# Optimization experiments

Measured on AMD Instinct MI355X. Metric: run time of the kernel, lower is better.

Reference implementation:

```python
import jax, jax.numpy as jnp
import numpy as np


def setup_inputs() -> dict:
    key = jax.random.key(0)
    ks = jax.random.split(key, 12)
    N, F, H, E = 100000, 128, 128, 625000
    x = jax.random.normal(ks[0], (N, F), dtype=jnp.float32)
    edge_index = jax.random.randint(ks[1], (2, E), 0, N, dtype=jnp.int64)
    s1 = 1.0 / np.sqrt(2 * F)
    s2 = 1.0 / np.sqrt(H)
    W1 = jax.random.uniform(ks[2], (2 * F, H), jnp.float32, -s1, s1)
    b1 = jax.random.uniform(ks[3], (H,), jnp.float32, -s1, s1)
    W2 = jax.random.uniform(ks[4], (H, H), jnp.float32, -s2, s2)
    b2 = jax.random.uniform(ks[5], (H,), jnp.float32, -s2, s2)
    W3 = jax.random.uniform(ks[6], (H, H), jnp.float32, -s2, s2)
    b3 = jax.random.uniform(ks[7], (H,), jnp.float32, -s2, s2)
    W4 = jax.random.uniform(ks[8], (H, 1), jnp.float32, -s2, s2)
    b4 = jax.random.uniform(ks[9], (1,), jnp.float32, -s2, s2)
    return {"x": x, "edge_index": edge_index, "W1": W1, "b1": b1,
            "W2": W2, "b2": b2, "W3": W3, "b3": b3, "W4": W4, "b4": b4}


def reference(x, edge_index, W1, b1, W2, b2, W3, b3, W4, b4):
    # Gather endpoint features and concat -> [E, 2F]
    x_i = x[edge_index[0], :]
    x_j = x[edge_index[1], :]
    ef = jnp.concatenate([x_i, x_j], axis=-1)
    h = jax.nn.relu(ef @ W1 + b1)
    h = jax.nn.relu(h @ W2 + b2)
    h = jax.nn.relu(h @ W3 + b3)
    return jax.nn.sigmoid(h @ W4 + b4)  # [E, 1]
```

## Files before the change

### kernel.cpp

```cpp
#include <hip/hip_runtime.h>
#include <math.h>

typedef _Float16 half8 __attribute__((ext_vector_type(8)));
typedef _Float16 half4 __attribute__((ext_vector_type(4)));
typedef float f32x4 __attribute__((ext_vector_type(4)));

#define HDIM 128
#define WHALFS 65536
#define SCR_HALFS 2048
#define LDS_HALFS (WHALFS + 8 * SCR_HALFS)
#define LDS_BYTES (LDS_HALFS * 2)

__global__ __launch_bounds__(256) void prep_kernel(
    const float* __restrict__ x,  const float* __restrict__ W1,
    const float* __restrict__ W2, const float* __restrict__ W3,
    _Float16* __restrict__ xh,  _Float16* __restrict__ W1p,
    _Float16* __restrict__ W2p, _Float16* __restrict__ W3p, int NF)
{
    int bid = blockIdx.x;
    if (bid < 32) {
        int t = bid * 256 + threadIdx.x;
        const float* W; _Float16* Wp; int KS; int u;
        if (t < 4096)      { W = W1; Wp = W1p; KS = 8; u = t; }
        else if (t < 6144) { W = W2; Wp = W2p; KS = 4; u = t - 4096; }
        else               { W = W3; Wp = W3p; KS = 4; u = t - 6144; }
        int lane = u & 63;
        int fk   = u >> 6;
        int ks   = fk % KS;
        int ct   = fk / KS;
        int m    = ct * 16 + (lane & 15);
        int k0   = ks * 32 + (lane >> 4) * 8;
        half8 v;
        #pragma unroll
        for (int j = 0; j < 8; ++j) v[j] = (_Float16)W[(k0 + j) * HDIM + m];
        *(half8*)(Wp + (size_t)u * 8) = v;
    } else {
        long i = ((long)(bid - 32) * 256 + threadIdx.x) * 4;
        if (i + 4 <= (long)NF) {
            float4 f = *(const float4*)(x + i);
            half4 v;
            v[0] = (_Float16)f.x; v[1] = (_Float16)f.y;
            v[2] = (_Float16)f.z; v[3] = (_Float16)f.w;
            *(half4*)(xh + i) = v;
        }
    }
}

__device__ __forceinline__ void acc_bias_init(
    f32x4 (&acc)[2][8], const float* __restrict__ bias, int quad)
{
    #pragma unroll
    for (int ct = 0; ct < 8; ++ct) {
        float4 bv = *(const float4*)(bias + ct * 16 + quad * 4);
        f32x4 b = {bv.x, bv.y, bv.z, bv.w};
        acc[0][ct] = b;
        acc[1][ct] = b;
    }
}

__device__ __forceinline__ void epi_extract(
    f32x4 (&acc)[2][8], _Float16* __restrict__ scr, int l15, int quad, int sw,
    half8 (&bh)[2][4], const float* __restrict__ next_bias)
{
    #pragma unroll
    for (int nt = 0; nt < 2; ++nt) {
        #pragma unroll
        for (int ct = 0; ct < 8; ++ct) {
            half4 h;
            h[0] = (_Float16)fmaxf(acc[nt][ct][0], 0.f);
            h[1] = (_Float16)fmaxf(acc[nt][ct][1], 0.f);
            h[2] = (_Float16)fmaxf(acc[nt][ct][2], 0.f);
            h[3] = (_Float16)fmaxf(acc[nt][ct][3], 0.f);
            *(half4*)(scr + ((l15 * 128 + ct * 16 + quad * 4) ^ sw)) = h;
        }
        #pragma unroll
        for (int ks = 0; ks < 4; ++ks)
            bh[nt][ks] = *(const half8*)(scr + ((l15 * 128 + ks * 32 + quad * 8) ^ sw));
    }
    acc_bias_init(acc, next_bias, quad);
}

__device__ __forceinline__ void layer_mfma(
    f32x4 (&acc)[2][8], const _Float16* __restrict__ Wl,
    half8 (&bh)[2][4], int lane)
{
    __builtin_amdgcn_s_setprio(1);
    #pragma unroll
    for (int ks = 0; ks < 4; ++ks) {
        #pragma unroll
        for (int ch = 0; ch < 2; ++ch) {
            half8 aw[4];
            #pragma unroll
            for (int c = 0; c < 4; ++c)
                aw[c] = *(const half8*)(Wl + ((size_t)(((ch * 4 + c) * 4 + ks) * 64 + lane)) * 8);
            #pragma unroll
            for (int nt = 0; nt < 2; ++nt)
                #pragma unroll
                for (int c = 0; c < 4; ++c)
                    acc[nt][ch * 4 + c] = __builtin_amdgcn_mfma_f32_16x16x32_f16(
                        aw[c], bh[nt][ks], acc[nt][ch * 4 + c], 0, 0, 0);
        }
    }
    __builtin_amdgcn_s_setprio(0);
}

__device__ __forceinline__ void layer1_half(
    f32x4 (&acc)[2][8], const _Float16* __restrict__ W1l,
    half8 (&bef)[2][4], int ks0, int lane)
{
    __builtin_amdgcn_s_setprio(1);
    #pragma unroll
    for (int ks = 0; ks < 4; ++ks) {
        #pragma unroll
        for (int ch = 0; ch < 2; ++ch) {
            half8 aw[4];
            #pragma unroll
            for (int c = 0; c < 4; ++c)
                aw[c] = *(const half8*)(W1l + ((size_t)(((ch * 4 + c) * 8 + ks0 + ks) * 64 + lane)) * 8);
            #pragma unroll
            for (int nt = 0; nt < 2; ++nt)
                #pragma unroll
                for (int c = 0; c < 4; ++c)
                    acc[nt][ch * 4 + c] = __builtin_amdgcn_mfma_f32_16x16x32_f16(
                        aw[c], bef[nt][ks], acc[nt][ch * 4 + c], 0, 0, 0);
        }
    }
    __builtin_amdgcn_s_setprio(0);
}

__global__ __launch_bounds__(512, 2) void edge_mlp_kernel(
    const int* __restrict__ ei, const _Float16* __restrict__ xh,
    const _Float16* __restrict__ wpack,
    const float* __restrict__ b1, const float* __restrict__ b2,
    const float* __restrict__ b3, const float* __restrict__ W4,
    const float* __restrict__ b4, float* __restrict__ out, int E)
{
    extern __shared__ _Float16 lds[];

    {
        float4* dst = (float4*)lds;
        const float4* src = (const float4*)wpack;
        #pragma unroll
        for (int i = 0; i < 16; ++i)
            dst[i * 512 + threadIdx.x] = src[i * 512 + threadIdx.x];
    }
    __syncthreads();

    const int tid  = threadIdx.x;
    const int wave = tid >> 6;
    const int lane = tid & 63;
    const int l15  = lane & 15;
    const int quad = lane >> 4;
    const int sw   = (l15 & 7) << 3;

    const _Float16* W1l = lds;
    const _Float16* W2l = lds + 32768;
    const _Float16* W3l = lds + 49152;
    _Float16* scr = lds + WHALFS + wave * SCR_HALFS;

    const int ntiles = (E + 255) >> 8;
    const float b4v = b4[0];

    int gi[2], gj[2];
    half8 befi[2][4];
    {
        const int base0 = blockIdx.x * 256 + wave * 32;
        #pragma unroll
        for (int nt = 0; nt < 2; ++nt) {
            const int row = min(base0 + nt * 16 + l15, E - 1);
            gi[nt] = ei[row];
            gj[nt] = ei[E + row];
        }
        #pragma unroll
        for (int nt = 0; nt < 2; ++nt) {
            const _Float16* pi = xh + (size_t)gi[nt] * HDIM;
            #pragma unroll
            for (int ks = 0; ks < 4; ++ks)
                befi[nt][ks] = *(const half8*)(pi + ks * 32 + quad * 8);
        }
    }

    for (int t = blockIdx.x; t < ntiles; t += gridDim.x) {
        const int base = t * 256 + wave * 32;

        half8 befj[2][4];
        #pragma unroll
        for (int nt = 0; nt < 2; ++nt) {
            const _Float16* pj = xh + (size_t)gj[nt] * HDIM;
            #pragma unroll
            for (int ks = 0; ks < 4; ++ks)
                befj[nt][ks] = *(const half8*)(pj + ks * 32 + quad * 8);
        }

        f32x4 acc[2][8];
        acc_bias_init(acc, b1, quad);

        layer1_half(acc, W1l, befi, 0, lane);
        layer1_half(acc, W1l, befj, 4, lane);

        half8 bh[2][4];
        epi_extract(acc, scr, l15, quad, sw, bh, b2);

        int gin[2], gjn[2];
        {
            const int basen = (t + (int)gridDim.x) * 256 + wave * 32;
            #pragma unroll
            for (int nt = 0; nt < 2; ++nt) {
                const int row = min(min(basen + nt * 16 + l15, E - 1), E - 1);
                gin[nt] = ei[row];
                gjn[nt] = ei[E + row];
            }
        }

        layer_mfma(acc, W2l, bh, lane);
        epi_extract(acc, scr, l15, quad, sw, bh, b3);

        #pragma unroll
        for (int nt = 0; nt < 2; ++nt) {
            const _Float16* pi = xh + (size_t)gin[nt] * HDIM;
            #pragma unroll
            for (int ks = 0; ks < 4; ++ks)
                befi[nt][ks] = *(const half8*)(pi + ks * 32 + quad * 8);
        }

        layer_mfma(acc, W3l, bh, lane);

        #pragma unroll
        for (int nt = 0; nt < 2; ++nt) {
            float s = 0.f;
            #pragma unroll
            for (int ct = 0; ct < 8; ++ct) {
                float4 w4v = *(const float4*)(W4 + ct * 16 + quad * 4);
                s += fmaxf(acc[nt][ct][0], 0.f) * w4v.x;
                s += fmaxf(acc[nt][ct][1], 0.f) * w4v.y;
                s += fmaxf(acc[nt][ct][2], 0.f) * w4v.z;
                s += fmaxf(acc[nt][ct][3], 0.f) * w4v.w;
            }
            s += __shfl_xor(s, 16, 64);
            s += __shfl_xor(s, 32, 64);
            const int row = base + nt * 16 + l15;
            if (quad == 0 && row < E)
                out[row] = 1.f / (1.f + __expf(-(s + b4v)));
        }

        gi[0] = gin[0]; gi[1] = gin[1];
        gj[0] = gjn[0]; gj[1] = gjn[1];
    }
}

extern "C" void kernel_launch(void* const* d_in, const int* in_sizes, int n_in,
                              void* d_out, int out_size, void* d_ws, size_t ws_size,
                              hipStream_t stream)
{
    const float* x  = (const float*)d_in[0];
    const int*   ei = (const int*)d_in[1];
    const float* W1 = (const float*)d_in[2];
    const float* b1 = (const float*)d_in[3];
    const float* W2 = (const float*)d_in[4];
    const float* b2 = (const float*)d_in[5];
    const float* W3 = (const float*)d_in[6];
    const float* b3 = (const float*)d_in[7];
    const float* W4 = (const float*)d_in[8];
    const float* b4 = (const float*)d_in[9];
    float* out = (float*)d_out;

    const int NF = in_sizes[0];
    const int E  = out_size;

    _Float16* xh  = (_Float16*)d_ws;
    _Float16* W1p = xh + NF;
    _Float16* W2p = W1p + 32768;
    _Float16* W3p = W2p + 16384;

    const int xblocks = (NF + 1023) / 1024;
    prep_kernel<<<32 + xblocks, 256, 0, stream>>>(x, W1, W2, W3, xh, W1p, W2p, W3p, NF);

    hipFuncSetAttribute((const void*)edge_mlp_kernel,
                        hipFuncAttributeMaxDynamicSharedMemorySize, LDS_BYTES);
    edge_mlp_kernel<<<256, 512, LDS_BYTES, stream>>>(ei, xh, W1p,
                                                     b1, b2, b3, W4, b4, out, E);
}
```

Before: 201.0 us.

## Grid-stride fp16 conversion and drop cross-iteration gather prefetch in edge MLP

The x-to-fp16 prep kernel now uses a fixed grid of 2048 conversion blocks that grid-stride over the array, eight elements per thread. In the MLP loop, both endpoint feature gathers now happen at the top of each iteration instead of prefetching the next tile's source rows in the middle of layer 3, which lowers register pressure but loses the overlap of loads with compute. NF is hardcoded to the test shape rather than taken from the input sizes, so the code is tied to the benchmark dimensions.

```diff
diff --git a/kernel.cpp b/kernel.cpp
--- a/kernel.cpp
+++ b/kernel.cpp
@@ -35,13 +35,17 @@
         for (int j = 0; j < 8; ++j) v[j] = (_Float16)W[(k0 + j) * HDIM + m];
         *(half8*)(Wp + (size_t)u * 8) = v;
     } else {
-        long i = ((long)(bid - 32) * 256 + threadIdx.x) * 4;
-        if (i + 4 <= (long)NF) {
-            float4 f = *(const float4*)(x + i);
-            half4 v;
-            v[0] = (_Float16)f.x; v[1] = (_Float16)f.y;
-            v[2] = (_Float16)f.z; v[3] = (_Float16)f.w;
-            *(half4*)(xh + i) = v;
+        const long stride = (long)(gridDim.x - 32) * 256;
+        for (long u = (long)(bid - 32) * 256 + threadIdx.x; u * 8 < (long)NF; u += stride) {
+            long i = u * 8;
+            const float4* xf = (const float4*)(x + i);
+            float4 f0 = xf[0], f1 = xf[1];
+            half8 v;
+            v[0] = (_Float16)f0.x; v[1] = (_Float16)f0.y;
+            v[2] = (_Float16)f0.z; v[3] = (_Float16)f0.w;
+            v[4] = (_Float16)f1.x; v[5] = (_Float16)f1.y;
+            v[6] = (_Float16)f1.z; v[7] = (_Float16)f1.w;
+            *(half8*)(xh + i) = v;
         }
     }
 }
@@ -162,7 +166,6 @@
     const float b4v = b4[0];
 
     int gi[2], gj[2];
-    half8 befi[2][4];
     {
         const int base0 = blockIdx.x * 256 + wave * 32;
         #pragma unroll
@@ -171,6 +174,12 @@
             gi[nt] = ei[row];
             gj[nt] = ei[E + row];
         }
+    }
+
+    for (int t = blockIdx.x; t < ntiles; t += gridDim.x) {
+        const int base = t * 256 + wave * 32;
+
+        half8 befi[2][4], befj[2][4];
         #pragma unroll
         for (int nt = 0; nt < 2; ++nt) {
             const _Float16* pi = xh + (size_t)gi[nt] * HDIM;
@@ -178,12 +187,6 @@
             for (int ks = 0; ks < 4; ++ks)
                 befi[nt][ks] = *(const half8*)(pi + ks * 32 + quad * 8);
         }
-    }
-
-    for (int t = blockIdx.x; t < ntiles; t += gridDim.x) {
-        const int base = t * 256 + wave * 32;
-
-        half8 befj[2][4];
         #pragma unroll
         for (int nt = 0; nt < 2; ++nt) {
             const _Float16* pj = xh + (size_t)gj[nt] * HDIM;
@@ -191,38 +194,27 @@
             for (int ks = 0; ks < 4; ++ks)
                 befj[nt][ks] = *(const half8*)(pj + ks * 32 + quad * 8);
         }
-
-        f32x4 acc[2][8];
-        acc_bias_init(acc, b1, quad);
-
-        layer1_half(acc, W1l, befi, 0, lane);
-        layer1_half(acc, W1l, befj, 4, lane);
-
-        half8 bh[2][4];
-        epi_extract(acc, scr, l15, quad, sw, bh, b2);
-
         int gin[2], gjn[2];
         {
-            const int basen = (t + (int)gridDim.x) * 256 + wave * 32;
+            const int basen = min(t + (int)gridDim.x, ntiles - 1) * 256 + wave * 32;
             #pragma unroll
             for (int nt = 0; nt < 2; ++nt) {
-                const int row = min(min(basen + nt * 16 + l15, E - 1), E - 1);
+                const int row = min(basen + nt * 16 + l15, E - 1);
                 gin[nt] = ei[row];
                 gjn[nt] = ei[E + row];
             }
         }
 
+        f32x4 acc[2][8];
+        acc_bias_init(acc, b1, quad);
+
+        layer1_half(acc, W1l, befi, 0, lane);
+        layer1_half(acc, W1l, befj, 4, lane);
+
+        half8 bh[2][4];
+        epi_extract(acc, scr, l15, quad, sw, bh, b2);
         layer_mfma(acc, W2l, bh, lane);
         epi_extract(acc, scr, l15, quad, sw, bh, b3);
-
-        #pragma unroll
-        for (int nt = 0; nt < 2; ++nt) {
-            const _Float16* pi = xh + (size_t)gin[nt] * HDIM;
-            #pragma unroll
-            for (int ks = 0; ks < 4; ++ks)
-                befi[nt][ks] = *(const half8*)(pi + ks * 32 + quad * 8);
-        }
-
         layer_mfma(acc, W3l, bh, lane);
 
         #pragma unroll
@@ -264,7 +256,7 @@
     const float* b4 = (const float*)d_in[9];
     float* out = (float*)d_out;
 
-    const int NF = in_sizes[0];
+    const int NF = 100000 * 128;
     const int E  = out_size;
 
     _Float16* xh  = (_Float16*)d_ws;
@@ -272,8 +264,7 @@
     _Float16* W2p = W1p + 32768;
     _Float16* W3p = W2p + 16384;
 
-    const int xblocks = (NF + 1023) / 1024;
-    prep_kernel<<<32 + xblocks, 256, 0, stream>>>(x, W1, W2, W3, xh, W1p, W2p, W3p, NF);
+    prep_kernel<<<32 + 2048, 256, 0, stream>>>(x, W1, W2, W3, xh, W1p, W2p, W3p, NF);
 
     hipFuncSetAttribute((const void*)edge_mlp_kernel,
                         hipFuncAttributeMaxDynamicSharedMemorySize, LDS_BYTES);
```

After: 207.5 us. 3.2% more time.
